# Kernel optimization log

Measured on AMD Instinct MI355X. Metric: run time of the kernel, lower is better.

The kernel has to match this reference:

```python
import jax, jax.numpy as jnp
import numpy as np

EPS = 1e-10
PHI = (1.0 + np.sqrt(5.0)) / 2.0
TAU = 2.0 * np.pi
LOG_CUTOFF = float(np.log(PHI ** 2))  # log(lambda_cutoff)


def _log_abs_diff(la, lb, same_sign):
    # log|a - b| (same sign) or log(|a| + |b|) (opposite sign), all in log space
    hi = jnp.maximum(la, lb)
    lo = jnp.minimum(la, lb)
    d = jnp.minimum(lo - hi, -1e-7)  # guard log1p(-1) on the (masked) diagonal
    log_diff = hi + jnp.log1p(-jnp.exp(d))
    log_sum = jnp.logaddexp(la, lb)
    return jnp.where(same_sign, log_diff, log_sum)


def log_cartesian_distance(ell1, theta1, ell2, theta2):
    # elementwise / broadcasting version of compute_log_cartesian_distance
    cos1, sin1 = jnp.cos(theta1), jnp.sin(theta1)
    cos2, sin2 = jnp.cos(theta2), jnp.sin(theta2)
    lx1 = ell1 + jnp.log(jnp.abs(cos1) + EPS)
    ly1 = ell1 + jnp.log(jnp.abs(sin1) + EPS)
    lx2 = ell2 + jnp.log(jnp.abs(cos2) + EPS)
    ly2 = ell2 + jnp.log(jnp.abs(sin2) + EPS)
    same_x = (jnp.sign(cos1) * jnp.sign(cos2)) > 0
    same_y = (jnp.sign(sin1) * jnp.sign(sin2)) > 0
    ldx = _log_abs_diff(lx1, lx2, same_x)
    ldy = _log_abs_diff(ly1, ly2, same_y)
    # 0.5 * logsumexp(2*ldx, 2*ldy) == log sqrt(dx^2 + dy^2)
    return 0.5 * jnp.logaddexp(2.0 * ldx, 2.0 * ldy)


def setup_inputs() -> dict:
    N = 4096
    key = jax.random.key(0)
    k1, k2 = jax.random.split(key)
    ell = jax.random.uniform(k1, (N,), dtype=jnp.float32) * np.float32(np.log(PHI ** 3))
    theta = jax.random.uniform(k2, (N,), dtype=jnp.float32) * np.float32(TAU)
    s = jnp.ones((N,), dtype=jnp.float32)
    frozen = jnp.zeros((N,), dtype=bool)
    return {"ell": ell, "theta": theta, "s": s, "frozen": frozen}


def reference(ell, theta, s, frozen):
    # compute_repulsion_direct: all-pairs log-distance repulsion with phi^2 cutoff
    N = ell.shape[0]
    # pairwise log distances: [N, N]
    ld = log_cartesian_distance(ell[:, None], theta[:, None], ell[None, :], theta[None, :])
    pair_mask = (ld <= LOG_CUTOFF) & (~jnp.eye(N, dtype=bool)) & (~frozen)[:, None]
    force = s[:, None] * s[None, :] * jnp.exp(-ld)  # s_i * s_j / dist
    force = jnp.where(pair_mask, force, jnp.zeros((), force.dtype))
    d_theta = jnp.mod(theta[None, :] - theta[:, None] + np.float32(np.pi), np.float32(TAU)) - np.float32(np.pi)
    d_ell = ell[None, :] - ell[:, None]
    F_ell = jnp.sum(force * d_ell, axis=1)
    F_theta = jnp.sum(force * d_theta, axis=1)
    return jnp.stack([F_ell, F_theta])  # [2, N]
```

## Files before the change

### kernel.cpp

```cpp
#include <hip/hip_runtime.h>
#include <math.h>

#define BLOCK 256
#define IPB 4

#define PI_F      3.14159265358979323846f
#define TAU_F     6.2831853071795864769f
#define INV_TAU_F 0.15915494309189533577f
#define PHI4_F    6.854101966249685f

extern "C" __device__ float __builtin_amdgcn_rsqf(float);

__global__ void precompute_kernel(const float* __restrict__ ell,
                                  const float* __restrict__ theta,
                                  float4* __restrict__ A, int n) {
    int i = blockIdx.x * blockDim.x + threadIdx.x;
    if (i < n) {
        float e = ell[i];
        float th = theta[i];
        float lam = expf(e);
        float sn, cs;
        sincosf(th, &sn, &cs);
        A[i] = make_float4(lam * cs, lam * sn, e, th);
    }
}

__global__ __launch_bounds__(BLOCK) void repulse_kernel(
        const float4* __restrict__ A,
        const float* __restrict__ s,
        const unsigned char* __restrict__ frozen,
        float* __restrict__ out, int n) {
    const int t  = threadIdx.x;
    const int i0 = blockIdx.x * IPB;

    float xi[IPB], yi[IPB], eli[IPB], api[IPB];
    int   iv[IPB];
#pragma unroll
    for (int v = 0; v < IPB; ++v) {
        int i = i0 + v;
        iv[v] = i;
        float4 a = A[i];
        xi[v] = a.x; yi[v] = a.y; eli[v] = a.z;
        api[v] = PI_F - a.w;
    }

    float Fe[IPB], Ft[IPB];
#pragma unroll
    for (int v = 0; v < IPB; ++v) { Fe[v] = 0.0f; Ft[v] = 0.0f; }

#pragma unroll 4
    for (int j = t; j < n; j += BLOCK) {
        float4 b = A[j];
        float sj = s[j];
#pragma unroll
        for (int v = 0; v < IPB; ++v) {
            float dx = b.x - xi[v];
            float dy = b.y - yi[v];
            float r2 = fmaf(dx, dx, dy * dy);
            float rinv = __builtin_amdgcn_rsqf(fmaxf(r2, 1e-30f));
            bool ok = (r2 <= PHI4_F) && (j != iv[v]);
            float f = ok ? sj * rinv : 0.0f;
            float tt = b.w + api[v];
            float dth = fmaf(-floorf(tt * INV_TAU_F), TAU_F, tt) - PI_F;
            Fe[v] = fmaf(f, b.z - eli[v], Fe[v]);
            Ft[v] = fmaf(f, dth, Ft[v]);
        }
    }

#pragma unroll
    for (int v = 0; v < IPB; ++v) {
#pragma unroll
        for (int off = 32; off >= 1; off >>= 1) {
            Fe[v] += __shfl_xor(Fe[v], off, 64);
            Ft[v] += __shfl_xor(Ft[v], off, 64);
        }
    }

    __shared__ float red[(BLOCK / 64) * IPB * 2];
    const int wave = t >> 6;
    const int lane = t & 63;
    if (lane == 0) {
#pragma unroll
        for (int v = 0; v < IPB; ++v) {
            red[wave * IPB * 2 + v * 2 + 0] = Fe[v];
            red[wave * IPB * 2 + v * 2 + 1] = Ft[v];
        }
    }
    __syncthreads();

    if (t < IPB * 2) {
        int v  = t >> 1;
        int c  = t & 1;
        float sum = 0.0f;
#pragma unroll
        for (int w = 0; w < BLOCK / 64; ++w)
            sum += red[w * IPB * 2 + v * 2 + c];
        int i = i0 + v;
        float val = frozen[i] ? 0.0f : s[i] * sum;
        out[c * n + i] = val;
    }
}

extern "C" void kernel_launch(void* const* d_in, const int* in_sizes, int n_in,
                              void* d_out, int out_size, void* d_ws, size_t ws_size,
                              hipStream_t stream) {
    const float* ell   = (const float*)d_in[0];
    const float* theta = (const float*)d_in[1];
    const float* s     = (const float*)d_in[2];
    const unsigned char* frozen = (const unsigned char*)d_in[3];
    float* out = (float*)d_out;
    int n = in_sizes[0];

    float4* A = (float4*)d_ws;

    int pre_blocks = (n + BLOCK - 1) / BLOCK;
    precompute_kernel<<<pre_blocks, BLOCK, 0, stream>>>(ell, theta, A, n);

    int grid = (n + IPB - 1) / IPB;
    repulse_kernel<<<grid, BLOCK, 0, stream>>>(A, s, frozen, out, n);
}
```

Measured before the change: 69.84 us.

## Fuse precompute into repulsion kernel, recomputing Cartesian coords on the fly

Removes the separate precompute launch and its float4 workspace. Each block now loads ell and theta directly and recomputes exp, sin and cos per j element with fast intrinsics. The diagonal check becomes r2>0 instead of comparing indices, and the clamp before rsq is dropped. This saves one launch and the workspace round trip, but adds redundant transcendental work in the inner loop (once per j per block) and uses lower-precision __expf and __sincosf.

```diff
diff --git a/kernel.cpp b/kernel.cpp
--- a/kernel.cpp
+++ b/kernel.cpp
@@ -11,22 +11,9 @@
 
 extern "C" __device__ float __builtin_amdgcn_rsqf(float);
 
-__global__ void precompute_kernel(const float* __restrict__ ell,
-                                  const float* __restrict__ theta,
-                                  float4* __restrict__ A, int n) {
-    int i = blockIdx.x * blockDim.x + threadIdx.x;
-    if (i < n) {
-        float e = ell[i];
-        float th = theta[i];
-        float lam = expf(e);
-        float sn, cs;
-        sincosf(th, &sn, &cs);
-        A[i] = make_float4(lam * cs, lam * sn, e, th);
-    }
-}
-
-__global__ __launch_bounds__(BLOCK) void repulse_kernel(
-        const float4* __restrict__ A,
+__global__ __launch_bounds__(BLOCK) void repulse_fused(
+        const float* __restrict__ ell,
+        const float* __restrict__ theta,
         const float* __restrict__ s,
         const unsigned char* __restrict__ frozen,
         float* __restrict__ out, int n) {
@@ -34,14 +21,17 @@
     const int i0 = blockIdx.x * IPB;
 
     float xi[IPB], yi[IPB], eli[IPB], api[IPB];
-    int   iv[IPB];
 #pragma unroll
     for (int v = 0; v < IPB; ++v) {
         int i = i0 + v;
-        iv[v] = i;
-        float4 a = A[i];
-        xi[v] = a.x; yi[v] = a.y; eli[v] = a.z;
-        api[v] = PI_F - a.w;
+        float e  = ell[i];
+        float th = theta[i];
+        float lam = __expf(e);
+        float sn, cs;
+        __sincosf(th, &sn, &cs);
+        xi[v] = lam * cs; yi[v] = lam * sn;
+        eli[v] = e;
+        api[v] = PI_F - th;
     }
 
     float Fe[IPB], Ft[IPB];
@@ -50,19 +40,24 @@
 
 #pragma unroll 4
     for (int j = t; j < n; j += BLOCK) {
-        float4 b = A[j];
+        float e  = ell[j];
+        float th = theta[j];
         float sj = s[j];
+        float lam = __expf(e);
+        float sn, cs;
+        __sincosf(th, &sn, &cs);
+        float bx = lam * cs, by = lam * sn;
 #pragma unroll
         for (int v = 0; v < IPB; ++v) {
-            float dx = b.x - xi[v];
-            float dy = b.y - yi[v];
+            float dx = bx - xi[v];
+            float dy = by - yi[v];
             float r2 = fmaf(dx, dx, dy * dy);
-            float rinv = __builtin_amdgcn_rsqf(fmaxf(r2, 1e-30f));
-            bool ok = (r2 <= PHI4_F) && (j != iv[v]);
+            float rinv = __builtin_amdgcn_rsqf(r2);
+            bool ok = (r2 <= PHI4_F) && (r2 > 0.0f);
             float f = ok ? sj * rinv : 0.0f;
-            float tt = b.w + api[v];
+            float tt = th + api[v];
             float dth = fmaf(-floorf(tt * INV_TAU_F), TAU_F, tt) - PI_F;
-            Fe[v] = fmaf(f, b.z - eli[v], Fe[v]);
+            Fe[v] = fmaf(f, e - eli[v], Fe[v]);
             Ft[v] = fmaf(f, dth, Ft[v]);
         }
     }
@@ -89,8 +84,8 @@
     __syncthreads();
 
     if (t < IPB * 2) {
-        int v  = t >> 1;
-        int c  = t & 1;
+        int v = t >> 1;
+        int c = t & 1;
         float sum = 0.0f;
 #pragma unroll
         for (int w = 0; w < BLOCK / 64; ++w)
@@ -111,11 +106,6 @@
     float* out = (float*)d_out;
     int n = in_sizes[0];
 
-    float4* A = (float4*)d_ws;
-
-    int pre_blocks = (n + BLOCK - 1) / BLOCK;
-    precompute_kernel<<<pre_blocks, BLOCK, 0, stream>>>(ell, theta, A, n);
-
     int grid = (n + IPB - 1) / IPB;
-    repulse_kernel<<<grid, BLOCK, 0, stream>>>(A, s, frozen, out, n);
+    repulse_fused<<<grid, BLOCK, 0, stream>>>(ell, theta, s, frozen, out, n);
 }
```

Result: no change. 68.82 us (-1.5%).
